# Optimization experiments

Hardware: AMD Instinct MI355X
Metric: run time of the kernel (lower is better)

The kernel has to match this reference:

```python
import jax, jax.numpy as jnp
import numpy as np
from jax import lax

BETA = 0.25            # commitment_beta (multiplies code_book_loss per source)
CODEBOOK_WEIGHT = 1.0  # multiplies commitment_loss per source
GN_GROUPS = 8
GN_EPS = 1e-5


def conv2d(x, w, b):
    # 3x3 same-padding conv, NCHW / OIHW
    y = lax.conv_general_dilated(x, w, (1, 1), [(1, 1), (1, 1)],
                                 dimension_numbers=('NCHW', 'OIHW', 'NCHW'))
    return y + b[None, :, None, None]


def group_norm(x, scale, bias):
    B, C, H, W = x.shape
    xg = x.reshape(B, GN_GROUPS, C // GN_GROUPS, H, W)
    mean = xg.mean(axis=(2, 3, 4), keepdims=True)
    var = xg.var(axis=(2, 3, 4), keepdims=True)
    xg = (xg - mean) * lax.rsqrt(var + GN_EPS)
    x = xg.reshape(B, C, H, W)
    return x * scale[None, :, None, None] + bias[None, :, None, None]


def setup_inputs() -> dict:
    key = jax.random.key(0)
    ks = jax.random.split(key, 4)
    x = jax.random.normal(ks[0], (8, 3, 64, 64), jnp.float32)
    conv_in_w = jax.random.normal(ks[1], (64, 3, 3, 3), jnp.float32) * 0.1
    conv_in_b = jnp.zeros((64,), jnp.float32)
    codebook = jax.random.normal(ks[2], (4096, 64), jnp.float32) * 0.5
    gn_scale = jnp.ones((64,), jnp.float32)
    gn_bias = jnp.zeros((64,), jnp.float32)
    dec_w = jax.random.normal(ks[3], (3, 64, 3, 3), jnp.float32) * 0.1
    dec_b = jnp.zeros((3,), jnp.float32)
    return {"x": x, "conv_in_w": conv_in_w, "conv_in_b": conv_in_b,
            "codebook": codebook, "gn_scale": gn_scale, "gn_bias": gn_bias,
            "dec_w": dec_w, "dec_b": dec_b}


def reference(x, conv_in_w, conv_in_b, codebook, gn_scale, gn_bias, dec_w, dec_b):
    # Encoder: channels=[64], mid_layers=[64] => just conv_in
    feat = conv2d(x, conv_in_w, conv_in_b)          # [B,64,H,W]
    B, C, H, W = feat.shape

    # quantize(): cdist -> argmin -> gather -> losses -> straight-through
    quant_in = feat.transpose(0, 2, 3, 1).reshape(B, H * W, C)  # [B,n,C]
    # squared euclidean distances (argmin identical to torch.cdist p=2 argmin)
    d = ((quant_in ** 2).sum(-1, keepdims=True)
         - 2.0 * jnp.einsum('bnc,kc->bnk', quant_in, codebook)
         + (codebook ** 2).sum(-1)[None, None, :])              # [B,n,K]
    min_idx = jnp.argmin(d, axis=-1)                            # [B,n]
    quant_out = codebook[min_idx.reshape(-1)]                   # [B*n,C]
    qi_flat = quant_in.reshape(-1, C)                            # [B*n,C]

    commitment_loss = CODEBOOK_WEIGHT * jnp.mean(
        (lax.stop_gradient(quant_out) - qi_flat) ** 2)
    code_book_loss = BETA * jnp.mean(
        (lax.stop_gradient(qi_flat) - quant_out) ** 2)

    st = qi_flat + lax.stop_gradient(quant_out - qi_flat)        # straight-through
    quant_nchw = st.reshape(B, H, W, C).transpose(0, 3, 1, 2)

    # Decoder: channels=[64] => norm_out + silu + decoder_out
    out = group_norm(quant_nchw, gn_scale, gn_bias)
    out = jax.nn.silu(out)
    reconstruction = conv2d(out, dec_w, dec_b)                   # [B,3,H,W]
    return reconstruction, quant_nchw, commitment_loss, code_book_loss
```

## Files before the change

kernel.cpp:

```cpp
#include <hip/hip_runtime.h>
#include <hip/hip_bf16.h>

typedef __attribute__((ext_vector_type(8))) short short8;
typedef __attribute__((ext_vector_type(4))) float f32x4;

#define KK 4096
#define NELEM 2097152
#define TAU 2.5e-4f

__device__ __forceinline__ unsigned short f2bf(float f) {
    unsigned u = __float_as_uint(f);
    u = (u + 0x7FFFu + ((u >> 16) & 1u)) >> 16;
    return (unsigned short)u;
}
__device__ __forceinline__ float bf2f(unsigned short h) {
    return __uint_as_float(((unsigned)h) << 16);
}

__global__ void k_prep(const float* __restrict__ cb, float* __restrict__ cn,
                       unsigned short* __restrict__ cbh, unsigned short* __restrict__ cbl,
                       int* __restrict__ wszero) {
    if (blockIdx.x == 0) {
        for (int i = threadIdx.x; i < 256; i += 256) wszero[i] = 0;
    }
    int t = blockIdx.x * 256 + threadIdx.x;
    int row = t >> 2, part = t & 3;
    const float4* p = (const float4*)(cb + (size_t)row * 64 + part * 16);
    float s = 0.f;
    short8 hv[2], lv[2];
#pragma unroll
    for (int i = 0; i < 4; i++) {
        float4 v = p[i];
        float arr[4] = {v.x, v.y, v.z, v.w};
#pragma unroll
        for (int j = 0; j < 4; j++) {
            float f = arr[j];
            s += f * f;
            int e = i * 4 + j;
            unsigned short h = f2bf(f);
            hv[e >> 3][e & 7] = (short)h;
            lv[e >> 3][e & 7] = (short)f2bf(f - bf2f(h));
        }
    }
    short8* oh = (short8*)(cbh + (size_t)row * 64 + part * 16);
    short8* ol = (short8*)(cbl + (size_t)row * 64 + part * 16);
    oh[0] = hv[0]; oh[1] = hv[1];
    ol[0] = lv[0]; ol[1] = lv[1];
    s += __shfl_xor(s, 1, 64);
    s += __shfl_xor(s, 2, 64);
    if (part == 0) cn[row] = s;
}

#define MFMA __builtin_amdgcn_mfma_f32_16x16x32_bf16

__global__ __launch_bounds__(256, 2) void k_argmin_part(
    const float* __restrict__ x, const float* __restrict__ ciw, const float* __restrict__ cib,
    const unsigned short* __restrict__ cbh, const unsigned short* __restrict__ cbl,
    const float* __restrict__ cn,
    float* __restrict__ pb1, float* __restrict__ pb2, int* __restrict__ pbi) {

    __shared__ float    slab[3][3][66];
    __shared__ unsigned qtile[64][65];
    __shared__ float    mb1[4][64];
    __shared__ float    mb2[4][64];
    __shared__ int      mi1[4][64];

    const int tid = threadIdx.x;
    const int L   = tid & 63;
    const int wv  = tid >> 6;
    const int blk = blockIdx.x;
    const int grp = blk >> 1, half = blk & 1;
    const int b   = grp >> 6, h = grp & 63;

    for (int idx = tid; idx < 594; idx += 256) {
        int ci = idx / 198, rem = idx - ci * 198;
        int kh = rem / 66,  colp = rem - kh * 66;
        int hh = h + kh - 1, ww = colp - 1;
        float v = 0.f;
        if (hh >= 0 && hh < 64 && ww >= 0 && ww < 64)
            v = x[((b * 3 + ci) << 12) + (hh << 6) + ww];
        slab[ci][kh][colp] = v;
    }
    __syncthreads();

    {
        const int w_  = L;
        const int cgs = __builtin_amdgcn_readfirstlane(wv);
        float xv[27];
#pragma unroll
        for (int ci = 0; ci < 3; ci++)
#pragma unroll
            for (int kh = 0; kh < 3; kh++)
#pragma unroll
                for (int kw = 0; kw < 3; kw++)
                    xv[ci * 9 + kh * 3 + kw] = slab[ci][kh][w_ + kw];
#pragma unroll
        for (int j = 0; j < 16; j++) {
            int co = cgs * 16 + j;
            float acc = cib[co];
#pragma unroll
            for (int t2 = 0; t2 < 27; t2++)
                acc = fmaf(xv[t2], ciw[co * 27 + t2], acc);
            unsigned short hbits = f2bf(acc);
            unsigned short lbits = f2bf(acc - bf2f(hbits));
            qtile[w_][co] = (unsigned)hbits | ((unsigned)lbits << 16);
        }
    }
    __syncthreads();

    const int col = L & 15, g = L >> 4;
    short8 qh[4][2], ql[4][2];
#pragma unroll
    for (int mt = 0; mt < 4; mt++) {
        int qrow = mt * 16 + col;
#pragma unroll
        for (int kh = 0; kh < 2; kh++) {
            int d0 = (kh * 4 + g) * 8;
#pragma unroll
            for (int e = 0; e < 8; e++) {
                unsigned u = qtile[qrow][d0 + e];
                qh[mt][kh][e] = (short)(u & 0xFFFFu);
                ql[mt][kh][e] = (short)(u >> 16);
            }
        }
    }

    float vb1[4][4], vb2[4][4];
    int   vi1[4][4];
#pragma unroll
    for (int mt = 0; mt < 4; mt++)
#pragma unroll
        for (int e = 0; e < 4; e++) { vb1[mt][e] = 3.4e38f; vb2[mt][e] = 3.4e38f; vi1[mt][e] = 0; }

    const int cbase0 = (half << 11) + (wv << 9);
    const unsigned short* ph = cbh + (size_t)(cbase0 + col) * 64;
    const unsigned short* pl = cbl + (size_t)(cbase0 + col) * 64;
    const float* pcn = cn + cbase0 + col;

    short8 c0h0, c0h1, c0l0, c0l1, c1h0, c1h1, c1l0, c1l1;
    float  cn0, cn1;

    auto LD = [&](int gi, short8& h0, short8& h1, short8& l0, short8& l1, float& cnv) {
        const short8* p0 = (const short8*)(ph + ((size_t)gi << 10));
        const short8* p1 = (const short8*)(pl + ((size_t)gi << 10));
        h0 = p0[g]; h1 = p0[4 + g]; l0 = p1[g]; l1 = p1[4 + g];
        cnv = pcn[gi << 4];
    };
    auto PROC = [&](int gi, short8& h0, short8& h1, short8& l0, short8& l1, float cnv) {
        int kvb = cbase0 + gi * 16 + col;
#pragma unroll
        for (int mt = 0; mt < 4; mt++) {
            f32x4 acc = {0.f, 0.f, 0.f, 0.f};
            acc = MFMA(qh[mt][0], h0, acc, 0, 0, 0);
            acc = MFMA(qh[mt][1], h1, acc, 0, 0, 0);
            acc = MFMA(qh[mt][0], l0, acc, 0, 0, 0);
            acc = MFMA(qh[mt][1], l1, acc, 0, 0, 0);
            acc = MFMA(ql[mt][0], h0, acc, 0, 0, 0);
            acc = MFMA(ql[mt][1], h1, acc, 0, 0, 0);
#pragma unroll
            for (int e = 0; e < 4; e++) {
                float s = fmaf(acc[e], -2.f, cnv);
                vb2[mt][e] = __builtin_amdgcn_fmed3f(s, vb1[mt][e], vb2[mt][e]);
                bool take = s < vb1[mt][e];
                vi1[mt][e] = take ? kvb : vi1[mt][e];
                vb1[mt][e] = take ? s : vb1[mt][e];
            }
        }
    };

    LD(0, c0h0, c0h1, c0l0, c0l1, cn0);
#pragma unroll 1
    for (int gi = 0; gi < 32; gi += 2) {
        LD(gi + 1, c1h0, c1h1, c1l0, c1l1, cn1);
        PROC(gi, c0h0, c0h1, c0l0, c0l1, cn0);
        int gn = gi + 2 <= 31 ? gi + 2 : 31;
        LD(gn, c0h0, c0h1, c0l0, c0l1, cn0);
        PROC(gi + 1, c1h0, c1h1, c1l0, c1l1, cn1);
    }

#pragma unroll
    for (int mt = 0; mt < 4; mt++)
#pragma unroll
    for (int e = 0; e < 4; e++) {
        float b1 = vb1[mt][e], b2 = vb2[mt][e];
        int i1 = vi1[mt][e];
#pragma unroll
        for (int m = 1; m < 16; m <<= 1) {
            float ob1 = __shfl_xor(b1, m, 64);
            float ob2 = __shfl_xor(b2, m, 64);
            int   oi1 = __shfl_xor(i1, m, 64);
            float hi = fmaxf(b1, ob1);
            b2 = fminf(fminf(b2, ob2), hi);
            bool take = (ob1 < b1) || ((ob1 == b1) && (oi1 < i1));
            if (take) { b1 = ob1; i1 = oi1; }
        }
        if (col == 0) {
            int qloc = mt * 16 + g * 4 + e;
            mb1[wv][qloc] = b1; mb2[wv][qloc] = b2; mi1[wv][qloc] = i1;
        }
    }
    __syncthreads();

    if (tid < 64) {
        float b1 = mb1[0][tid], b2 = mb2[0][tid];
        int i1 = mi1[0][tid];
#pragma unroll
        for (int w2 = 1; w2 < 4; w2++) {
            float ob1 = mb1[w2][tid], ob2 = mb2[w2][tid];
            int   oi1 = mi1[w2][tid];
            float hi = fmaxf(b1, ob1);
            b2 = fminf(fminf(b2, ob2), hi);
            bool take = (ob1 < b1) || ((ob1 == b1) && (oi1 < i1));
            if (take) { b1 = ob1; i1 = oi1; }
        }
        int o = (blk << 6) + tid;
        pb1[o] = b1; pb2[o] = b2; pbi[o] = i1;
    }
}

__global__ __launch_bounds__(256, 2) void k_merge(
    const float* __restrict__ x, const float* __restrict__ ciw, const float* __restrict__ cib,
    const float* __restrict__ cb, const float* __restrict__ cn,
    const float* __restrict__ pb1, const float* __restrict__ pb2, const int* __restrict__ pbi,
    float* __restrict__ quant, float* __restrict__ ssd,
    float* __restrict__ gsum, float* __restrict__ gsq) {

    __shared__ float slab[3][3][66];
    __shared__ float qf32[64][65];
    __shared__ int   fi[64];
    __shared__ float gred[4][16];
    __shared__ int   nflag;
    __shared__ int   flagged[64];
    __shared__ float rb[4];
    __shared__ int   ri[4];

    const int tid = threadIdx.x;
    const int L   = tid & 63;
    const int wv  = tid >> 6;
    const int grp = blockIdx.x;
    const int b   = grp >> 6, h = grp & 63;

    if (tid == 0) nflag = 0;
    for (int idx = tid; idx < 594; idx += 256) {
        int ci = idx / 198, rem = idx - ci * 198;
        int kh = rem / 66,  colp = rem - kh * 66;
        int hh = h + kh - 1, ww = colp - 1;
        float v = 0.f;
        if (hh >= 0 && hh < 64 && ww >= 0 && ww < 64)
            v = x[((b * 3 + ci) << 12) + (hh << 6) + ww];
        slab[ci][kh][colp] = v;
    }
    __syncthreads();
    {
        const int w_  = L;
        const int cgs = __builtin_amdgcn_readfirstlane(wv);
        float xv[27];
#pragma unroll
        for (int ci = 0; ci < 3; ci++)
#pragma unroll
            for (int kh = 0; kh < 3; kh++)
#pragma unroll
                for (int kw = 0; kw < 3; kw++)
                    xv[ci * 9 + kh * 3 + kw] = slab[ci][kh][w_ + kw];
#pragma unroll
        for (int j = 0; j < 16; j++) {
            int co = cgs * 16 + j;
            float acc = cib[co];
#pragma unroll
            for (int t2 = 0; t2 < 27; t2++)
                acc = fmaf(xv[t2], ciw[co * 27 + t2], acc);
            qf32[w_][co] = acc;
        }
    }
    __syncthreads();

    if (tid < 64) {
        int i0 = (grp << 7) + tid;
        int j0 = i0 + 64;
        float b1 = pb1[i0], b2 = pb2[i0];
        int   i1 = pbi[i0];
        float ob1 = pb1[j0], ob2 = pb2[j0];
        int   oi1 = pbi[j0];
        float hi = fmaxf(b1, ob1);
        b2 = fminf(fminf(b2, ob2), hi);
        bool take = (ob1 < b1) || ((ob1 == b1) && (oi1 < i1));
        if (take) { b1 = ob1; i1 = oi1; }
        fi[tid] = i1;
        if (b2 - b1 < TAU) {
            int p = atomicAdd(&nflag, 1);
            flagged[p] = tid;
        }
    }
    __syncthreads();

    int nf = nflag;
    for (int r = 0; r < nf; r++) {
        int qf = flagged[r];
        float best = 3.4e38f; int bi = 0;
        for (int kk = 0; kk < 16; kk++) {
            int k = kk * 256 + tid;
            const float4* cp = (const float4*)(cb + (size_t)k * 64);
            float d0 = 0.f, d1 = 0.f, d2 = 0.f, d3 = 0.f;
#pragma unroll
            for (int i = 0; i < 16; i += 4) {
                float4 c0 = cp[i], c1 = cp[i+1], c2 = cp[i+2], c3 = cp[i+3];
                d0 += qf32[qf][4*i+ 0]*c0.x + qf32[qf][4*i+ 1]*c0.y + qf32[qf][4*i+ 2]*c0.z + qf32[qf][4*i+ 3]*c0.w;
                d1 += qf32[qf][4*i+ 4]*c1.x + qf32[qf][4*i+ 5]*c1.y + qf32[qf][4*i+ 6]*c1.z + qf32[qf][4*i+ 7]*c1.w;
                d2 += qf32[qf][4*i+ 8]*c2.x + qf32[qf][4*i+ 9]*c2.y + qf32[qf][4*i+10]*c2.z + qf32[qf][4*i+11]*c2.w;
                d3 += qf32[qf][4*i+12]*c3.x + qf32[qf][4*i+13]*c3.y + qf32[qf][4*i+14]*c3.z + qf32[qf][4*i+15]*c3.w;
            }
            float s = cn[k] - 2.f * ((d0 + d1) + (d2 + d3));
            if (s < best) { best = s; bi = k; }
        }
#pragma unroll
        for (int off = 32; off; off >>= 1) {
            float ob = __shfl_down(best, off, 64);
            int   oi = __shfl_down(bi, off, 64);
            if (ob < best || (ob == best && oi < bi)) { best = ob; bi = oi; }
        }
        if (L == 0) { rb[wv] = best; ri[wv] = bi; }
        __syncthreads();
        if (tid == 0) {
            float bb = rb[0]; int ii = ri[0];
#pragma unroll
            for (int w2 = 1; w2 < 4; w2++)
                if (rb[w2] < bb || (rb[w2] == bb && ri[w2] < ii)) { bb = rb[w2]; ii = ri[w2]; }
            fi[qf] = ii;
        }
        __syncthreads();
    }

    {
        int qloc = tid >> 2, part = tid & 3;
        int idx = fi[qloc];
        int q = (grp << 6) + qloc;
        int hw = q & 4095;
        const float* crow = cb + (size_t)idx * 64 + part * 16;
        float* qout = quant + ((size_t)b << 18) + ((size_t)(part * 16) << 12) + hw;
        float ps = 0.f, sA = 0.f, sA2 = 0.f, sB = 0.f, sB2 = 0.f;
#pragma unroll
        for (int cc = 0; cc < 16; cc++) {
            float fv = qf32[qloc][part * 16 + cc];
            float cv = crow[cc];
            float d = cv - fv;
            ps += d * d;
            if (cc < 8) { sA += cv; sA2 += cv * cv; } else { sB += cv; sB2 += cv * cv; }
            qout[(size_t)cc << 12] = cv;
        }
#pragma unroll
        for (int off = 32; off; off >>= 1) ps += __shfl_down(ps, off, 64);
        if (L == 0) atomicAdd(ssd, ps);
#pragma unroll
        for (int m = 4; m <= 32; m <<= 1) {
            sA  += __shfl_xor(sA, m, 64);  sA2 += __shfl_xor(sA2, m, 64);
            sB  += __shfl_xor(sB, m, 64);  sB2 += __shfl_xor(sB2, m, 64);
        }
        if (L < 4) {
            gred[wv][L * 4 + 0] = sA;  gred[wv][L * 4 + 1] = sA2;
            gred[wv][L * 4 + 2] = sB;  gred[wv][L * 4 + 3] = sB2;
        }
    }
    __syncthreads();
    if (tid < 16) {
        float v = gred[0][tid] + gred[1][tid] + gred[2][tid] + gred[3][tid];
        int part = tid >> 2, stat = tid & 3;
        int g2 = b * 8 + part * 2 + (stat >> 1);
        atomicAdd((stat & 1) ? &gsq[g2] : &gsum[g2], v);
    }
}

__global__ __launch_bounds__(256, 2) void k_out(
    const float* __restrict__ quant,
    const float* __restrict__ gsum, const float* __restrict__ gsq,
    const float* __restrict__ scale, const float* __restrict__ bias,
    const float* __restrict__ dw, const float* __restrict__ db,
    const float* __restrict__ ssd, float* __restrict__ losses,
    float* __restrict__ out) {

    __shared__ float nls[64 * 3 * 66];
    __shared__ float sc_s[64], bi_s[64];

    const int tid = threadIdx.x;
    const int blk = blockIdx.x;
    const int b = blk >> 6, h = blk & 63;

    if (blk == 0 && tid == 0) {
        float mean = ssd[0] / 2097152.f;
        losses[0] = mean;
        losses[1] = 0.25f * mean;
    }

    if (tid < 64) {
        int grp = b * 8 + (tid >> 3);
        float m = gsum[grp] * (1.f / 32768.f);
        float var = gsq[grp] * (1.f / 32768.f) - m * m;
        float r = rsqrtf(var + 1e-5f);
        float sc = scale[tid] * r;
        sc_s[tid] = sc;
        bi_s[tid] = bias[tid] - m * sc;
    }
    for (int idx = tid; idx < 384; idx += 256) {
        int ci = idx / 6, r2 = idx % 6;
        int kh = r2 >> 1, side = r2 & 1;
        nls[ci * 198 + kh * 66 + (side ? 65 : 0)] = 0.f;
    }
    __syncthreads();

#pragma unroll
    for (int i = 0; i < 48; i++) {
        int idx = tid + i * 256;
        int w_ = idx & 63;
        int t2 = idx >> 6;
        int kh = t2 % 3, ci = t2 / 3;
        int hh = h + kh - 1;
        float v = 0.f;
        if (hh >= 0 && hh < 64) {
            float qv = quant[((size_t)(b * 64 + ci) << 12) + (hh << 6) + w_];
            float y = qv * sc_s[ci] + bi_s[ci];
            v = y / (1.f + expf(-y));
        }
        nls[ci * 198 + kh * 66 + w_ + 1] = v;
    }
    __syncthreads();

    const int co = tid >> 6;
    const int w_ = tid & 63;
    if (co < 3) {
        float acc = db[co];
#pragma unroll 4
        for (int ci = 0; ci < 64; ci++) {
            const float* wt = dw + (size_t)(co * 64 + ci) * 9;
#pragma unroll
            for (int kh = 0; kh < 3; kh++) {
                const float* base = nls + ci * 198 + kh * 66 + w_;
                acc = fmaf(base[0], wt[kh * 3 + 0], acc);
                acc = fmaf(base[1], wt[kh * 3 + 1], acc);
                acc = fmaf(base[2], wt[kh * 3 + 2], acc);
            }
        }
        out[((size_t)(b * 3 + co) << 12) + (h << 6) + w_] = acc;
    }
}

extern "C" void kernel_launch(void* const* d_in, const int* in_sizes, int n_in,
                              void* d_out, int out_size, void* d_ws, size_t ws_size,
                              hipStream_t stream) {
    const float* x   = (const float*)d_in[0];
    const float* ciw = (const float*)d_in[1];
    const float* cib = (const float*)d_in[2];
    const float* cb  = (const float*)d_in[3];
    const float* gsc = (const float*)d_in[4];
    const float* gbi = (const float*)d_in[5];
    const float* dw  = (const float*)d_in[6];
    const float* db  = (const float*)d_in[7];

    float* out = (float*)d_out;
    char* wsb  = (char*)d_ws;

    float*          ssd  = (float*)wsb;
    float*          gsum = (float*)(wsb + 64);
    float*          gsq  = (float*)(wsb + 320);
    float*          cn   = (float*)(wsb + 4096);
    unsigned short* cbh  = (unsigned short*)(wsb + 131072);
    unsigned short* cbl  = (unsigned short*)(wsb + 655360);
    float*          pb1  = (float*)(wsb + 1179648);
    float*          pb2  = (float*)(wsb + 1441792);
    int*            pbi  = (int*)(wsb + 1703936);

    float* recon  = out;
    float* quant  = out + 98304;
    float* losses = out + 98304 + NELEM;

    k_prep        <<<64,   256, 0, stream>>>(cb, cn, cbh, cbl, (int*)wsb);
    k_argmin_part <<<1024, 256, 0, stream>>>(x, ciw, cib, cbh, cbl, cn, pb1, pb2, pbi);
    k_merge       <<<512,  256, 0, stream>>>(x, ciw, cib, cb, cn, pb1, pb2, pbi,
                                             quant, ssd, gsum, gsq);
    k_out         <<<512,  256, 0, stream>>>(quant, gsum, gsq, gsc, gbi, dw, db,
                                             ssd, losses, recon);
}
```

Before: 289.6 us.

## Fuse partial argmin and merge kernels into a single full-codebook argmin kernel

Each block now scans the whole codebook with four waves of 1024 codes each, instead of splitting it across two blocks and merging in a second kernel. This drops the partial-result buffers, one kernel launch, and the recomputation of the input conv in the merge kernel. The cost is half as many blocks, each doing twice the MFMA work, plus extra shared memory for the fp32 tile, which may reduce parallelism or occupancy.

Measured after the change: 272.0 us. -6.1%, faster.

```diff
diff --git a/kernel.cpp b/kernel.cpp
--- a/kernel.cpp
+++ b/kernel.cpp
@@ -53,186 +53,25 @@
 
 #define MFMA __builtin_amdgcn_mfma_f32_16x16x32_bf16
 
-__global__ __launch_bounds__(256, 2) void k_argmin_part(
+__global__ __launch_bounds__(256, 2) void k_argmin(
     const float* __restrict__ x, const float* __restrict__ ciw, const float* __restrict__ cib,
     const unsigned short* __restrict__ cbh, const unsigned short* __restrict__ cbl,
-    const float* __restrict__ cn,
-    float* __restrict__ pb1, float* __restrict__ pb2, int* __restrict__ pbi) {
+    const float* __restrict__ cn, const float* __restrict__ cb,
+    float* __restrict__ quant, float* __restrict__ ssd,
+    float* __restrict__ gsum, float* __restrict__ gsq) {
 
     __shared__ float    slab[3][3][66];
     __shared__ unsigned qtile[64][65];
+    __shared__ float    qf32[64][65];
     __shared__ float    mb1[4][64];
     __shared__ float    mb2[4][64];
     __shared__ int      mi1[4][64];
-
-    const int tid = threadIdx.x;
-    const int L   = tid & 63;
-    const int wv  = tid >> 6;
-    const int blk = blockIdx.x;
-    const int grp = blk >> 1, half = blk & 1;
-    const int b   = grp >> 6, h = grp & 63;
-
-    for (int idx = tid; idx < 594; idx += 256) {
-        int ci = idx / 198, rem = idx - ci * 198;
-        int kh = rem / 66,  colp = rem - kh * 66;
-        int hh = h + kh - 1, ww = colp - 1;
-        float v = 0.f;
-        if (hh >= 0 && hh < 64 && ww >= 0 && ww < 64)
-            v = x[((b * 3 + ci) << 12) + (hh << 6) + ww];
-        slab[ci][kh][colp] = v;
-    }
-    __syncthreads();
-
-    {
-        const int w_  = L;
-        const int cgs = __builtin_amdgcn_readfirstlane(wv);
-        float xv[27];
-#pragma unroll
-        for (int ci = 0; ci < 3; ci++)
-#pragma unroll
-            for (int kh = 0; kh < 3; kh++)
-#pragma unroll
-                for (int kw = 0; kw < 3; kw++)
-                    xv[ci * 9 + kh * 3 + kw] = slab[ci][kh][w_ + kw];
-#pragma unroll
-        for (int j = 0; j < 16; j++) {
-            int co = cgs * 16 + j;
-            float acc = cib[co];
-#pragma unroll
-            for (int t2 = 0; t2 < 27; t2++)
-                acc = fmaf(xv[t2], ciw[co * 27 + t2], acc);
-            unsigned short hbits = f2bf(acc);
-            unsigned short lbits = f2bf(acc - bf2f(hbits));
-            qtile[w_][co] = (unsigned)hbits | ((unsigned)lbits << 16);
-        }
-    }
-    __syncthreads();
-
-    const int col = L & 15, g = L >> 4;
-    short8 qh[4][2], ql[4][2];
-#pragma unroll
-    for (int mt = 0; mt < 4; mt++) {
-        int qrow = mt * 16 + col;
-#pragma unroll
-        for (int kh = 0; kh < 2; kh++) {
-            int d0 = (kh * 4 + g) * 8;
-#pragma unroll
-            for (int e = 0; e < 8; e++) {
-                unsigned u = qtile[qrow][d0 + e];
-                qh[mt][kh][e] = (short)(u & 0xFFFFu);
-                ql[mt][kh][e] = (short)(u >> 16);
-            }
-        }
-    }
-
-    float vb1[4][4], vb2[4][4];
-    int   vi1[4][4];
-#pragma unroll
-    for (int mt = 0; mt < 4; mt++)
-#pragma unroll
-        for (int e = 0; e < 4; e++) { vb1[mt][e] = 3.4e38f; vb2[mt][e] = 3.4e38f; vi1[mt][e] = 0; }
-
-    const int cbase0 = (half << 11) + (wv << 9);
-    const unsigned short* ph = cbh + (size_t)(cbase0 + col) * 64;
-    const unsigned short* pl = cbl + (size_t)(cbase0 + col) * 64;
-    const float* pcn = cn + cbase0 + col;
-
-    short8 c0h0, c0h1, c0l0, c0l1, c1h0, c1h1, c1l0, c1l1;
-    float  cn0, cn1;
-
-    auto LD = [&](int gi, short8& h0, short8& h1, short8& l0, short8& l1, float& cnv) {
-        const short8* p0 = (const short8*)(ph + ((size_t)gi << 10));
-        const short8* p1 = (const short8*)(pl + ((size_t)gi << 10));
-        h0 = p0[g]; h1 = p0[4 + g]; l0 = p1[g]; l1 = p1[4 + g];
-        cnv = pcn[gi << 4];
-    };
-    auto PROC = [&](int gi, short8& h0, short8& h1, short8& l0, short8& l1, float cnv) {
-        int kvb = cbase0 + gi * 16 + col;
-#pragma unroll
-        for (int mt = 0; mt < 4; mt++) {
-            f32x4 acc = {0.f, 0.f, 0.f, 0.f};
-            acc = MFMA(qh[mt][0], h0, acc, 0, 0, 0);
-            acc = MFMA(qh[mt][1], h1, acc, 0, 0, 0);
-            acc = MFMA(qh[mt][0], l0, acc, 0, 0, 0);
-            acc = MFMA(qh[mt][1], l1, acc, 0, 0, 0);
-            acc = MFMA(ql[mt][0], h0, acc, 0, 0, 0);
-            acc = MFMA(ql[mt][1], h1, acc, 0, 0, 0);
-#pragma unroll
-            for (int e = 0; e < 4; e++) {
-                float s = fmaf(acc[e], -2.f, cnv);
-                vb2[mt][e] = __builtin_amdgcn_fmed3f(s, vb1[mt][e], vb2[mt][e]);
-                bool take = s < vb1[mt][e];
-                vi1[mt][e] = take ? kvb : vi1[mt][e];
-                vb1[mt][e] = take ? s : vb1[mt][e];
-            }
-        }
-    };
-
-    LD(0, c0h0, c0h1, c0l0, c0l1, cn0);
-#pragma unroll 1
-    for (int gi = 0; gi < 32; gi += 2) {
-        LD(gi + 1, c1h0, c1h1, c1l0, c1l1, cn1);
-        PROC(gi, c0h0, c0h1, c0l0, c0l1, cn0);
-        int gn = gi + 2 <= 31 ? gi + 2 : 31;
-        LD(gn, c0h0, c0h1, c0l0, c0l1, cn0);
-        PROC(gi + 1, c1h0, c1h1, c1l0, c1l1, cn1);
-    }
-
-#pragma unroll
-    for (int mt = 0; mt < 4; mt++)
-#pragma unroll
-    for (int e = 0; e < 4; e++) {
-        float b1 = vb1[mt][e], b2 = vb2[mt][e];
-        int i1 = vi1[mt][e];
-#pragma unroll
-        for (int m = 1; m < 16; m <<= 1) {
-            float ob1 = __shfl_xor(b1, m, 64);
-            float ob2 = __shfl_xor(b2, m, 64);
-            int   oi1 = __shfl_xor(i1, m, 64);
-            float hi = fmaxf(b1, ob1);
-            b2 = fminf(fminf(b2, ob2), hi);
-            bool take = (ob1 < b1) || ((ob1 == b1) && (oi1 < i1));
-            if (take) { b1 = ob1; i1 = oi1; }
-        }
-        if (col == 0) {
-            int qloc = mt * 16 + g * 4 + e;
-            mb1[wv][qloc] = b1; mb2[wv][qloc] = b2; mi1[wv][qloc] = i1;
-        }
-    }
-    __syncthreads();
-
-    if (tid < 64) {
-        float b1 = mb1[0][tid], b2 = mb2[0][tid];
-        int i1 = mi1[0][tid];
-#pragma unroll
-        for (int w2 = 1; w2 < 4; w2++) {
-            float ob1 = mb1[w2][tid], ob2 = mb2[w2][tid];
-            int   oi1 = mi1[w2][tid];
-            float hi = fmaxf(b1, ob1);
-            b2 = fminf(fminf(b2, ob2), hi);
-            bool take = (ob1 < b1) || ((ob1 == b1) && (oi1 < i1));
-            if (take) { b1 = ob1; i1 = oi1; }
-        }
-        int o = (blk << 6) + tid;
-        pb1[o] = b1; pb2[o] = b2; pbi[o] = i1;
-    }
-}
-
-__global__ __launch_bounds__(256, 2) void k_merge(
-    const float* __restrict__ x, const float* __restrict__ ciw, const float* __restrict__ cib,
-    const float* __restrict__ cb, const float* __restrict__ cn,
-    const float* __restrict__ pb1, const float* __restrict__ pb2, const int* __restrict__ pbi,
-    float* __restrict__ quant, float* __restrict__ ssd,
-    float* __restrict__ gsum, float* __restrict__ gsq) {
-
-    __shared__ float slab[3][3][66];
-    __shared__ float qf32[64][65];
-    __shared__ int   fi[64];
-    __shared__ float gred[4][16];
-    __shared__ int   nflag;
-    __shared__ int   flagged[64];
-    __shared__ float rb[4];
-    __shared__ int   ri[4];
+    __shared__ int      fi[64];
+    __shared__ float    gred[4][16];
+    __shared__ int      nflag;
+    __shared__ int      flagged[64];
+    __shared__ float    rb[4];
+    __shared__ int      ri[4];
 
     const int tid = threadIdx.x;
     const int L   = tid & 63;
@@ -251,6 +90,7 @@
         slab[ci][kh][colp] = v;
     }
     __syncthreads();
+
     {
         const int w_  = L;
         const int cgs = __builtin_amdgcn_readfirstlane(wv);
@@ -269,22 +109,119 @@
 #pragma unroll
             for (int t2 = 0; t2 < 27; t2++)
                 acc = fmaf(xv[t2], ciw[co * 27 + t2], acc);
-            qf32[w_][co] = acc;
+            unsigned short hbits = f2bf(acc);
+            unsigned short lbits = f2bf(acc - bf2f(hbits));
+            qf32[w_][co]  = acc;
+            qtile[w_][co] = (unsigned)hbits | ((unsigned)lbits << 16);
+        }
+    }
+    __syncthreads();
+
+    const int col = L & 15, g = L >> 4;
+    short8 qh[4][2], ql[4][2];
+#pragma unroll
+    for (int mt = 0; mt < 4; mt++) {
+        int qrow = mt * 16 + col;
+#pragma unroll
+        for (int kh = 0; kh < 2; kh++) {
+            int d0 = (kh * 4 + g) * 8;
+#pragma unroll
+            for (int e = 0; e < 8; e++) {
+                unsigned u = qtile[qrow][d0 + e];
+                qh[mt][kh][e] = (short)(u & 0xFFFFu);
+                ql[mt][kh][e] = (short)(u >> 16);
+            }
+        }
+    }
+
+    float vb1[4][4], vb2[4][4];
+    int   vi1[4][4];
+#pragma unroll
+    for (int mt = 0; mt < 4; mt++)
+#pragma unroll
+        for (int e = 0; e < 4; e++) { vb1[mt][e] = 3.4e38f; vb2[mt][e] = 3.4e38f; vi1[mt][e] = 0; }
+
+    const int cbase0 = wv << 10;
+    const unsigned short* ph = cbh + (size_t)(cbase0 + col) * 64;
+    const unsigned short* pl = cbl + (size_t)(cbase0 + col) * 64;
+    const float* pcn = cn + cbase0 + col;
+
+    short8 c0h0, c0h1, c0l0, c0l1, c1h0, c1h1, c1l0, c1l1;
+    float  cn0, cn1;
+
+    auto LD = [&](int gi, short8& h0, short8& h1, short8& l0, short8& l1, float& cnv) {
+        const short8* p0 = (const short8*)(ph + ((size_t)gi << 10));
+        const short8* p1 = (const short8*)(pl + ((size_t)gi << 10));
+        h0 = p0[g]; h1 = p0[4 + g]; l0 = p1[g]; l1 = p1[4 + g];
+        cnv = pcn[gi << 4];
+    };
+    auto PROC = [&](int gi, short8& h0, short8& h1, short8& l0, short8& l1, float cnv) {
+        int kvb = cbase0 + gi * 16 + col;
+#pragma unroll
+        for (int mt = 0; mt < 4; mt++) {
+            f32x4 acc = {0.f, 0.f, 0.f, 0.f};
+            acc = MFMA(qh[mt][0], h0, acc, 0, 0, 0);
+            acc = MFMA(qh[mt][1], h1, acc, 0, 0, 0);
+            acc = MFMA(qh[mt][0], l0, acc, 0, 0, 0);
+            acc = MFMA(qh[mt][1], l1, acc, 0, 0, 0);
+            acc = MFMA(ql[mt][0], h0, acc, 0, 0, 0);
+            acc = MFMA(ql[mt][1], h1, acc, 0, 0, 0);
+#pragma unroll
+            for (int e = 0; e < 4; e++) {
+                float s = fmaf(acc[e], -2.f, cnv);
+                vb2[mt][e] = __builtin_amdgcn_fmed3f(s, vb1[mt][e], vb2[mt][e]);
+                bool take = s < vb1[mt][e];
+                vi1[mt][e] = take ? kvb : vi1[mt][e];
+                vb1[mt][e] = take ? s : vb1[mt][e];
+            }
+        }
+    };
+
+    LD(0, c0h0, c0h1, c0l0, c0l1, cn0);
+#pragma unroll 1
+    for (int gi = 0; gi < 64; gi += 2) {
+        LD(gi + 1, c1h0, c1h1, c1l0, c1l1, cn1);
+        PROC(gi, c0h0, c0h1, c0l0, c0l1, cn0);
+        int gn = gi + 2 <= 63 ? gi + 2 : 63;
+        LD(gn, c0h0, c0h1, c0l0, c0l1, cn0);
+        PROC(gi + 1, c1h0, c1h1, c1l0, c1l1, cn1);
+    }
+
+#pragma unroll
+    for (int mt = 0; mt < 4; mt++)
+#pragma unroll
+    for (int e = 0; e < 4; e++) {
+        float b1 = vb1[mt][e], b2 = vb2[mt][e];
+        int i1 = vi1[mt][e];
+#pragma unroll
+        for (int m = 1; m < 16; m <<= 1) {
+            float ob1 = __shfl_xor(b1, m, 64);
+            float ob2 = __shfl_xor(b2, m, 64);
+            int   oi1 = __shfl_xor(i1, m, 64);
+            float hi = fmaxf(b1, ob1);
+            b2 = fminf(fminf(b2, ob2), hi);
+            bool take = (ob1 < b1) || ((ob1 == b1) && (oi1 < i1));
+            if (take) { b1 = ob1; i1 = oi1; }
+        }
+        if (col == 0) {
+            int qloc = mt * 16 + g * 4 + e;
+            mb1[wv][qloc] = b1; mb2[wv][qloc] = b2; mi1[wv][qloc] = i1;
         }
     }
     __syncthreads();
 
     if (tid < 64) {
-        int i0 = (grp << 7) + tid;
-        int j0 = i0 + 64;
-        float b1 = pb1[i0], b2 = pb2[i0];
-        int   i1 = pbi[i0];
-        float ob1 = pb1[j0], ob2 = pb2[j0];
-        int   oi1 = pbi[j0];
-        float hi = fmaxf(b1, ob1);
-        b2 = fminf(fminf(b2, ob2), hi);
-        bool take = (ob1 < b1) || ((ob1 == b1) && (oi1 < i1));
-        if (take) { b1 = ob1; i1 = oi1; }
+        float b1 = mb1[0][tid], b2 = mb2[0][tid];
+        int i1 = mi1[0][tid];
+#pragma unroll
+        for (int w2 = 1; w2 < 4; w2++) {
+            float ob1 = mb1[w2][tid], ob2 = mb2[w2][tid];
+            int   oi1 = mi1[w2][tid];
+            float hi = fmaxf(b1, ob1);
+            b2 = fminf(fminf(b2, ob2), hi);
+            bool take = (ob1 < b1) || ((ob1 == b1) && (oi1 < i1));
+            if (take) { b1 = ob1; i1 = oi1; }
+        }
         fi[tid] = i1;
         if (b2 - b1 < TAU) {
             int p = atomicAdd(&nflag, 1);
@@ -463,18 +400,14 @@
     float*          cn   = (float*)(wsb + 4096);
     unsigned short* cbh  = (unsigned short*)(wsb + 131072);
     unsigned short* cbl  = (unsigned short*)(wsb + 655360);
-    float*          pb1  = (float*)(wsb + 1179648);
-    float*          pb2  = (float*)(wsb + 1441792);
-    int*            pbi  = (int*)(wsb + 1703936);
 
     float* recon  = out;
     float* quant  = out + 98304;
     float* losses = out + 98304 + NELEM;
 
-    k_prep        <<<64,   256, 0, stream>>>(cb, cn, cbh, cbl, (int*)wsb);
-    k_argmin_part <<<1024, 256, 0, stream>>>(x, ciw, cib, cbh, cbl, cn, pb1, pb2, pbi);
-    k_merge       <<<512,  256, 0, stream>>>(x, ciw, cib, cb, cn, pb1, pb2, pbi,
-                                             quant, ssd, gsum, gsq);
-    k_out         <<<512,  256, 0, stream>>>(quant, gsum, gsq, gsc, gbi, dw, db,
-                                             ssd, losses, recon);
-}
+    k_prep   <<<64,  256, 0, stream>>>(cb, cn, cbh, cbl, (int*)wsb);
+    k_argmin <<<512, 256, 0, stream>>>(x, ciw, cib, cbh, cbl, cn, cb,
+                                       quant, ssd, gsum, gsq);
+    k_out    <<<512, 256, 0, stream>>>(quant, gsum, gsq, gsc, gbi, dw, db,
+                                       ssd, losses, recon);
+}
```
